# Performance work log

Measured on AMD Instinct MI355X. Metric: run time of the kernel, lower is better.

The kernel has to match this reference:

```python
import jax, jax.numpy as jnp
import numpy as np

B, L = 2, 5            # batches (scenes) and cavs per scene (fixed record_len)
THRESHOLD = 0.01       # communication threshold (eval path)
K_SIZE, SIGMA = 5, 1.0 # fixed gaussian smoothing filter


def _gaussian_kernel():
    c = K_SIZE // 2
    xx, yy = np.mgrid[0 - c:K_SIZE - c, 0 - c:K_SIZE - c]
    k = 1.0 / (2.0 * np.pi * SIGMA) * np.exp(-(np.square(xx) + np.square(yy)) / (2.0 * SIGMA ** 2))
    return jnp.asarray(k, jnp.float32)[None, None]  # OIHW (1,1,k,k)


def setup_inputs() -> dict:
    key = jax.random.key(0)
    ks = jax.random.split(key, 9)
    N, C, H, W, A = B * L, 64, 128, 256, 2
    return {
        "x": jax.random.normal(ks[0], (N, C, H, W), jnp.float32),
        "psm_single": jax.random.normal(ks[1], (N, A, H, W), jnp.float32),
        "inv_delay": jax.random.uniform(ks[2], (N,), jnp.float32, 0.1, 5.0),
        "ew_w": jax.random.normal(ks[3], (1,), jnp.float32),
        "ew_b": jax.random.normal(ks[4], (1,), jnp.float32),
        "ewc_w": jax.random.normal(ks[5], (1,), jnp.float32),
        "ewc_b": jax.random.normal(ks[6], (1,), jnp.float32),
        "sta_w1": jax.random.normal(ks[7], (4, 64), jnp.float32) * 0.1,
        "sta_w2": jax.random.normal(ks[8], (64, 4), jnp.float32) * 0.1,
    }


def reference(x, psm_single, inv_delay, ew_w, ew_b, ewc_w, ewc_b, sta_w1, sta_w2):
    N, C, H, W = x.shape
    dt = x.dtype

    # EnhanceWeight: per-cav AoI gate tanh(fc(1/(delay+0.1))) + 1
    enw = jnp.tanh(inv_delay * ew_w[0] + ew_b[0]) + 1.0          # (N,)
    x = x * enw[:, None, None, None]

    # Communication: sigmoid confidence, max over anchors, AoI gate, gaussian smooth
    conf = jax.nn.sigmoid(psm_single).max(axis=1, keepdims=True)  # (N,1,H,W)
    enc = jnp.tanh(inv_delay * ewc_w[0] + ewc_b[0]) + 1.0
    conf = conf * enc[:, None, None, None]
    conf = jax.lax.conv_general_dilated(
        conf, _gaussian_kernel().astype(dt), (1, 1), 'SAME',
        dimension_numbers=('NCHW', 'OIHW', 'NCHW'))
    mask = (conf > THRESHOLD).astype(dt)                          # (N,1,H,W)
    mask = mask.reshape(B, L, 1, H, W).at[:, 0].set(1.0)          # ego always communicates
    comm_rate = mask.mean()

    xm = x.reshape(B, L, C, H, W) * mask                          # masked per-cav features

    # TransformerFusion: per-pixel cross-agent attention, keep ego (row 0) output only
    feats = xm.transpose(0, 3, 4, 1, 2).reshape(B, H * W, L, C)   # (B, P, L, C)
    scale = 1.0 / jnp.sqrt(jnp.asarray(C, dt))
    scores = jnp.einsum('bpc,bplc->bpl', feats[:, :, 0], feats) * scale
    attn = jax.nn.softmax(scores, axis=-1)                        # (B, P, L)
    fused = jnp.einsum('bpl,bplc->bpc', attn, feats)              # (B, P, C)
    x_fuse = fused.transpose(0, 2, 1).reshape(B, C, H, W)

    # ShortTermAttention: channel gate from shared MLP over avg- and max-pooled stats
    def fc(v):  # v: (B, C)
        return jax.nn.relu(v @ sta_w1.T) @ sta_w2.T

    avg = x_fuse.mean(axis=(2, 3))
    mx = x_fuse.max(axis=(2, 3))
    gate = jax.nn.sigmoid(fc(avg) + fc(mx))                       # (B, C)
    out = x_fuse * gate[:, :, None, None]
    return out, comm_rate
```

## Files before the change

### kernel.cpp

```cpp
#include <hip/hip_runtime.h>
#include <math.h>

#define BB 2
#define LL 5
#define NN 10
#define CC 64
#define HH 128
#define WW 256
#define PP (HH*WW)
#define NP (NN*PP)


__global__ __launch_bounds__(256) void k_confmask(const float* __restrict__ psm,
                                                  const float* __restrict__ inv_delay,
                                                  const float* __restrict__ ewc_w,
                                                  const float* __restrict__ ewc_b,
                                                  float* __restrict__ mask,
                                                  float* __restrict__ cntp) {
    const float g0 = 0.15915494309189535f;
    const float g1 = 0.09653235263005391f;
    const float g2 = 0.05854983152431917f;
    const float g4 = 0.02153927930184936f;
    const float g5 = 0.01306423328468446f;
    const float g8 = 0.00291502449738744f;
    const float G[25] = { g8,g5,g4,g5,g8,
                          g5,g2,g1,g2,g5,
                          g4,g1,g0,g1,g4,
                          g5,g2,g1,g2,g5,
                          g8,g5,g4,g5,g8 };
    int blk = blockIdx.x;
    int n   = blk >> 7;
    int h   = blk & 127;
    int t   = threadIdx.x;
    float enc = tanhf(inv_delay[n] * ewc_w[0] + ewc_b[0]) + 1.0f;
    const float* pn0 = psm + (n * 2 + 0) * PP;
    const float* pn1 = psm + (n * 2 + 1) * PP;

    __shared__ float cs[5][WW];
#pragma unroll
    for (int r = 0; r < 5; ++r) {
        int row = h - 2 + r;
        float v = 0.0f;
        if ((unsigned)row < (unsigned)HH) {
            float a0 = pn0[row * WW + t];
            float a1 = pn1[row * WW + t];
            v = fmaxf(1.0f / (1.0f + expf(-a0)), 1.0f / (1.0f + expf(-a1))) * enc;
        }
        cs[r][t] = v;
    }
    __syncthreads();

    float acc = 0.0f;
#pragma unroll
    for (int r = 0; r < 5; ++r) {
#pragma unroll
        for (int dx = -2; dx <= 2; ++dx) {
            int col = t + dx;
            if ((unsigned)col < (unsigned)WW)
                acc += cs[r][col] * G[r * 5 + (dx + 2)];
        }
    }
    float mv = (acc > 0.01f) ? 1.0f : 0.0f;
    if ((n % LL) == 0) mv = 1.0f;
    mask[n * PP + h * WW + t] = mv;

    float v = mv;
#pragma unroll
    for (int o = 32; o > 0; o >>= 1) v += __shfl_down(v, o, 64);
    __shared__ float sred[4];
    int lane = t & 63, wid = t >> 6;
    if (lane == 0) sred[wid] = v;
    __syncthreads();
    if (t == 0) cntp[blk] = sred[0] + sred[1] + sred[2] + sred[3];
}

__global__ __launch_bounds__(256) void k_attnfuse(const float* __restrict__ x,
                                                  const float* __restrict__ mask,
                                                  const float* __restrict__ inv_delay,
                                                  const float* __restrict__ ew_w,
                                                  const float* __restrict__ ew_b,
                                                  float* __restrict__ out) {
    int blk = blockIdx.x;
    int b   = blk >> 9;
    int lane = threadIdx.x & 63;
    int wv   = threadIdx.x >> 6;
    int p = ((blk & 511) << 6) + lane;
    const float* xb = x + b * (LL * CC * PP) + p;
    int cbase = wv << 4;

    float xr[16][5];
    float s5[5] = {0.f, 0.f, 0.f, 0.f, 0.f};
#pragma unroll
    for (int cc = 0; cc < 16; ++cc) {
        const float* xc = xb + (cbase + cc) * PP;
#pragma unroll
        for (int l = 0; l < LL; ++l) xr[cc][l] = xc[l * CC * PP];
        float q = xr[cc][0];
#pragma unroll
        for (int l = 0; l < LL; ++l) s5[l] += q * xr[cc][l];
    }

    __shared__ float sred[4][5][64];
#pragma unroll
    for (int l = 0; l < LL; ++l) sred[wv][l][lane] = s5[l];
    __syncthreads();

    float ew0 = ew_w[0], eb0 = ew_b[0];
    float a[5];
    {
        float m[5], t[5], sc[5], e[5];
#pragma unroll
        for (int l = 0; l < LL; ++l) {
            t[l] = sred[0][l][lane] + sred[1][l][lane] + sred[2][l][lane] + sred[3][l][lane];
            float en = tanhf(inv_delay[b * LL + l] * ew0 + eb0) + 1.0f;
            m[l] = en * mask[(b * LL + l) * PP + p];
        }
        const float scale = 0.125f;
#pragma unroll
        for (int l = 0; l < LL; ++l) sc[l] = t[l] * m[0] * m[l] * scale;
        float mxv = fmaxf(fmaxf(fmaxf(sc[0], sc[1]), fmaxf(sc[2], sc[3])), sc[4]);
        float sum = 0.f;
#pragma unroll
        for (int l = 0; l < LL; ++l) { e[l] = expf(sc[l] - mxv); sum += e[l]; }
        float inv = 1.0f / sum;
#pragma unroll
        for (int l = 0; l < LL; ++l) a[l] = e[l] * inv * m[l];
    }

    float* ob = out + b * (CC * PP) + p;
#pragma unroll
    for (int cc = 0; cc < 16; ++cc) {
        float f = 0.f;
#pragma unroll
        for (int l = 0; l < LL; ++l) f += a[l] * xr[cc][l];
        ob[(cbase + cc) * PP] = f;
    }
}

__global__ void k_reduce(const float* __restrict__ xfuse,
                         float* __restrict__ avg_part,
                         float* __restrict__ mx_part) {
    int blk = blockIdx.x;
    int bc = blk >> 1;
    int half = blk & 1;
    const float4* row = (const float4*)(xfuse + bc * PP) + half * 4096;
    float s = 0.0f, m = -INFINITY;
    for (int i = threadIdx.x; i < 4096; i += 256) {
        float4 v = row[i];
        s += v.x + v.y + v.z + v.w;
        m = fmaxf(m, fmaxf(fmaxf(v.x, v.y), fmaxf(v.z, v.w)));
    }
#pragma unroll
    for (int o = 32; o > 0; o >>= 1) {
        s += __shfl_down(s, o, 64);
        m = fmaxf(m, __shfl_down(m, o, 64));
    }
    __shared__ float ss[4], sm[4];
    int lane = threadIdx.x & 63, wid = threadIdx.x >> 6;
    if (lane == 0) { ss[wid] = s; sm[wid] = m; }
    __syncthreads();
    if (threadIdx.x == 0) {
        avg_part[blk] = ss[0] + ss[1] + ss[2] + ss[3];
        mx_part[blk]  = fmaxf(fmaxf(sm[0], sm[1]), fmaxf(sm[2], sm[3]));
    }
}

__global__ __launch_bounds__(256) void k_scalegate(float* __restrict__ out,
                                                   const float* __restrict__ avg_part,
                                                   const float* __restrict__ mx_part,
                                                   const float* __restrict__ w1,
                                                   const float* __restrict__ w2,
                                                   const float* __restrict__ cntp) {
    int idx = blockIdx.x * 256 + threadIdx.x;
    int bc = idx >> 13;
    int b  = bc >> 6;
    int c  = bc & 63;
    __shared__ float hs[4];
    if (threadIdx.x < 4) {
        int j = threadIdx.x;
        float ha = 0.f, hm = 0.f;
        const float invP = 1.0f / (float)PP;
        for (int ch = 0; ch < CC; ++ch) {
            int i = (b * CC + ch) * 2;
            float av = (avg_part[i] + avg_part[i + 1]) * invP;
            float mv = fmaxf(mx_part[i], mx_part[i + 1]);
            float wv = w1[j * CC + ch];
            ha += av * wv;
            hm += mv * wv;
        }
        hs[j] = fmaxf(ha, 0.0f) + fmaxf(hm, 0.0f);
    }
    float4 v = ((float4*)out)[idx];
    __syncthreads();
    float g = hs[0] * w2[c * 4 + 0] + hs[1] * w2[c * 4 + 1]
            + hs[2] * w2[c * 4 + 2] + hs[3] * w2[c * 4 + 3];
    float gate = 1.0f / (1.0f + expf(-g));
    v.x *= gate; v.y *= gate; v.z *= gate; v.w *= gate;
    ((float4*)out)[idx] = v;

    if (blockIdx.x == 0) {
        float s = 0.0f;
        for (int j = threadIdx.x; j < 1280; j += 256) s += cntp[j];
#pragma unroll
        for (int o = 32; o > 0; o >>= 1) s += __shfl_down(s, o, 64);
        __shared__ float cs[4];
        int lane = threadIdx.x & 63, wid = threadIdx.x >> 6;
        if (lane == 0) cs[wid] = s;
        __syncthreads();
        if (threadIdx.x == 0)
            out[BB * CC * PP] = (cs[0] + cs[1] + cs[2] + cs[3]) * (1.0f / (float)NP);
    }
}

extern "C" void kernel_launch(void* const* d_in, const int* in_sizes, int n_in,
                              void* d_out, int out_size, void* d_ws, size_t ws_size,
                              hipStream_t stream) {
    const float* x         = (const float*)d_in[0];
    const float* psm       = (const float*)d_in[1];
    const float* inv_delay = (const float*)d_in[2];
    const float* ew_w      = (const float*)d_in[3];
    const float* ew_b      = (const float*)d_in[4];
    const float* ewc_w     = (const float*)d_in[5];
    const float* ewc_b     = (const float*)d_in[6];
    const float* w1        = (const float*)d_in[7];
    const float* w2        = (const float*)d_in[8];
    float* out = (float*)d_out;
    float* wsf = (float*)d_ws;

    float* avgp = wsf + 64;
    float* mxp  = wsf + 320;
    float* cntp = wsf + 576;
    float* mask = wsf + 4096;

    k_confmask<<<NN * HH, 256, 0, stream>>>(psm, inv_delay, ewc_w, ewc_b, mask, cntp);
    k_attnfuse<<<1024, 256, 0, stream>>>(x, mask, inv_delay, ew_w, ew_b, out);
    k_reduce<<<256, 256, 0, stream>>>(out, avgp, mxp);
    k_scalegate<<<BB * CC * PP / 4 / 256, 256, 0, stream>>>(out, avgp, mxp, w1, w2, cntp);
}
```

Before: 53.20 us.

## Fuse confidence mask and channel stats into attention kernel; split gate compute

Computes the gaussian-smoothed confidence mask for all five cavs directly inside the attention-fusion kernel using a shared-memory halo tile, which removes the mask buffer round trip and one launch. The same kernel also produces per-block channel sum and max partials through wave shuffles, so the separate pass that re-read the fused output for pooling is gone. A single-block finish kernel builds the gate and the comm rate, and a light scale kernel applies the gate. In exchange, psm halo regions are recomputed redundantly across blocks and each channel now pays a per-channel shuffle reduction.

Measured after the change: 56.10 us. 5.5% more time.

```diff
diff --git a/kernel.cpp b/kernel.cpp
--- a/kernel.cpp
+++ b/kernel.cpp
@@ -11,11 +11,16 @@
 #define NP (NN*PP)
 
 
-__global__ __launch_bounds__(256) void k_confmask(const float* __restrict__ psm,
+__global__ __launch_bounds__(256) void k_attnfuse(const float* __restrict__ x,
+                                                  const float* __restrict__ psm,
                                                   const float* __restrict__ inv_delay,
+                                                  const float* __restrict__ ew_w,
+                                                  const float* __restrict__ ew_b,
                                                   const float* __restrict__ ewc_w,
                                                   const float* __restrict__ ewc_b,
-                                                  float* __restrict__ mask,
+                                                  float* __restrict__ out,
+                                                  float* __restrict__ partS,
+                                                  float* __restrict__ partM,
                                                   float* __restrict__ cntp) {
     const float g0 = 0.15915494309189535f;
     const float g1 = 0.09653235263005391f;
@@ -28,63 +33,63 @@
                           g4,g1,g0,g1,g4,
                           g5,g2,g1,g2,g5,
                           g8,g5,g4,g5,g8 };
-    int blk = blockIdx.x;
-    int n   = blk >> 7;
-    int h   = blk & 127;
-    int t   = threadIdx.x;
-    float enc = tanhf(inv_delay[n] * ewc_w[0] + ewc_b[0]) + 1.0f;
-    const float* pn0 = psm + (n * 2 + 0) * PP;
-    const float* pn1 = psm + (n * 2 + 1) * PP;
-
-    __shared__ float cs[5][WW];
-#pragma unroll
-    for (int r = 0; r < 5; ++r) {
-        int row = h - 2 + r;
-        float v = 0.0f;
-        if ((unsigned)row < (unsigned)HH) {
-            float a0 = pn0[row * WW + t];
-            float a1 = pn1[row * WW + t];
-            v = fmaxf(1.0f / (1.0f + expf(-a0)), 1.0f / (1.0f + expf(-a1))) * enc;
-        }
-        cs[r][t] = v;
-    }
-    __syncthreads();
-
-    float acc = 0.0f;
-#pragma unroll
-    for (int r = 0; r < 5; ++r) {
-#pragma unroll
-        for (int dx = -2; dx <= 2; ++dx) {
-            int col = t + dx;
-            if ((unsigned)col < (unsigned)WW)
-                acc += cs[r][col] * G[r * 5 + (dx + 2)];
-        }
-    }
-    float mv = (acc > 0.01f) ? 1.0f : 0.0f;
-    if ((n % LL) == 0) mv = 1.0f;
-    mask[n * PP + h * WW + t] = mv;
-
-    float v = mv;
-#pragma unroll
-    for (int o = 32; o > 0; o >>= 1) v += __shfl_down(v, o, 64);
-    __shared__ float sred[4];
-    int lane = t & 63, wid = t >> 6;
-    if (lane == 0) sred[wid] = v;
-    __syncthreads();
-    if (t == 0) cntp[blk] = sred[0] + sred[1] + sred[2] + sred[3];
-}
-
-__global__ __launch_bounds__(256) void k_attnfuse(const float* __restrict__ x,
-                                                  const float* __restrict__ mask,
-                                                  const float* __restrict__ inv_delay,
-                                                  const float* __restrict__ ew_w,
-                                                  const float* __restrict__ ew_b,
-                                                  float* __restrict__ out) {
+
     int blk = blockIdx.x;
     int b   = blk >> 9;
-    int lane = threadIdx.x & 63;
-    int wv   = threadIdx.x >> 6;
-    int p = ((blk & 511) << 6) + lane;
+    int tid  = threadIdx.x;
+    int lane = tid & 63;
+    int wv   = tid >> 6;
+    int pblock = blk & 511;
+    int p = (pblock << 6) + lane;
+    int h  = pblock >> 2;
+    int c0 = (pblock & 3) << 6;
+
+    __shared__ float cs[5 * 5 * 68];
+    __shared__ float encs[5], enws[5];
+    if (tid < 5)
+        encs[tid] = tanhf(inv_delay[b * LL + tid] * ewc_w[0] + ewc_b[0]) + 1.0f;
+    else if (tid < 10)
+        enws[tid - 5] = tanhf(inv_delay[b * LL + tid - 5] * ew_w[0] + ew_b[0]) + 1.0f;
+    __syncthreads();
+
+    for (int idx = tid; idx < 1700; idx += 256) {
+        int l   = idx / 340;
+        int rem = idx - l * 340;
+        int r   = rem / 68;
+        int cc2 = rem - r * 68;
+        int row = h - 2 + r;
+        int col = c0 - 2 + cc2;
+        float v = 0.0f;
+        if ((unsigned)row < (unsigned)HH && (unsigned)col < (unsigned)WW) {
+            int n = b * LL + l;
+            float a0 = psm[(n * 2 + 0) * PP + row * WW + col];
+            float a1 = psm[(n * 2 + 1) * PP + row * WW + col];
+            v = fmaxf(1.0f / (1.0f + expf(-a0)), 1.0f / (1.0f + expf(-a1))) * encs[l];
+        }
+        cs[idx] = v;
+    }
+    __syncthreads();
+
+    float mv[5];
+#pragma unroll
+    for (int l = 0; l < LL; ++l) {
+        float acc = 0.0f;
+#pragma unroll
+        for (int r = 0; r < 5; ++r)
+#pragma unroll
+            for (int dx = 0; dx < 5; ++dx)
+                acc += cs[l * 340 + r * 68 + lane + dx] * G[r * 5 + dx];
+        mv[l] = (acc > 0.01f) ? 1.0f : 0.0f;
+    }
+    mv[0] = 1.0f;
+
+    if (wv == 0) {
+        float v = mv[0] + mv[1] + mv[2] + mv[3] + mv[4];
+#pragma unroll
+        for (int o = 32; o > 0; o >>= 1) v += __shfl_down(v, o, 64);
+        if (lane == 0) cntp[blk] = v;
+    }
+
     const float* xb = x + b * (LL * CC * PP) + p;
     int cbase = wv << 4;
 
@@ -105,15 +110,13 @@
     for (int l = 0; l < LL; ++l) sred[wv][l][lane] = s5[l];
     __syncthreads();
 
-    float ew0 = ew_w[0], eb0 = ew_b[0];
     float a[5];
     {
         float m[5], t[5], sc[5], e[5];
 #pragma unroll
         for (int l = 0; l < LL; ++l) {
             t[l] = sred[0][l][lane] + sred[1][l][lane] + sred[2][l][lane] + sred[3][l][lane];
-            float en = tanhf(inv_delay[b * LL + l] * ew0 + eb0) + 1.0f;
-            m[l] = en * mask[(b * LL + l) * PP + p];
+            m[l] = enws[l] * mv[l];
         }
         const float scale = 0.125f;
 #pragma unroll
@@ -134,82 +137,87 @@
 #pragma unroll
         for (int l = 0; l < LL; ++l) f += a[l] * xr[cc][l];
         ob[(cbase + cc) * PP] = f;
-    }
-}
-
-__global__ void k_reduce(const float* __restrict__ xfuse,
-                         float* __restrict__ avg_part,
-                         float* __restrict__ mx_part) {
-    int blk = blockIdx.x;
-    int bc = blk >> 1;
-    int half = blk & 1;
-    const float4* row = (const float4*)(xfuse + bc * PP) + half * 4096;
-    float s = 0.0f, m = -INFINITY;
-    for (int i = threadIdx.x; i < 4096; i += 256) {
-        float4 v = row[i];
-        s += v.x + v.y + v.z + v.w;
-        m = fmaxf(m, fmaxf(fmaxf(v.x, v.y), fmaxf(v.z, v.w)));
-    }
-#pragma unroll
-    for (int o = 32; o > 0; o >>= 1) {
-        s += __shfl_down(s, o, 64);
-        m = fmaxf(m, __shfl_down(m, o, 64));
-    }
-    __shared__ float ss[4], sm[4];
-    int lane = threadIdx.x & 63, wid = threadIdx.x >> 6;
-    if (lane == 0) { ss[wid] = s; sm[wid] = m; }
-    __syncthreads();
-    if (threadIdx.x == 0) {
-        avg_part[blk] = ss[0] + ss[1] + ss[2] + ss[3];
-        mx_part[blk]  = fmaxf(fmaxf(sm[0], sm[1]), fmaxf(sm[2], sm[3]));
-    }
-}
-
-__global__ __launch_bounds__(256) void k_scalegate(float* __restrict__ out,
-                                                   const float* __restrict__ avg_part,
-                                                   const float* __restrict__ mx_part,
-                                                   const float* __restrict__ w1,
-                                                   const float* __restrict__ w2,
-                                                   const float* __restrict__ cntp) {
+
+        float sv = f, mm = f;
+#pragma unroll
+        for (int o = 1; o < 64; o <<= 1) {
+            sv += __shfl_xor(sv, o, 64);
+            mm = fmaxf(mm, __shfl_xor(mm, o, 64));
+        }
+        if (lane == 0) {
+            partS[blk * CC + cbase + cc] = sv;
+            partM[blk * CC + cbase + cc] = mm;
+        }
+    }
+}
+
+__global__ __launch_bounds__(256) void k_finish(const float* __restrict__ partS,
+                                                const float* __restrict__ partM,
+                                                const float* __restrict__ cntp,
+                                                const float* __restrict__ w1,
+                                                const float* __restrict__ w2,
+                                                float* __restrict__ gate,
+                                                float* __restrict__ comm_out) {
+    int t = threadIdx.x;
+    int pair = t >> 1;
+    int sub  = t & 1;
+    __shared__ float sS[2][128], sM[2][128];
+    {
+        int b = pair >> 6, c = pair & 63;
+        float s = 0.f, m = -INFINITY;
+        int base = b * 512 + sub * 256;
+        for (int pb = 0; pb < 256; ++pb) {
+            int i = (base + pb) * CC + c;
+            s += partS[i];
+            m = fmaxf(m, partM[i]);
+        }
+        sS[sub][pair] = s;
+        sM[sub][pair] = m;
+    }
+    __syncthreads();
+    __shared__ float stA[128], stM[128];
+    if (t < 128) {
+        stA[t] = (sS[0][t] + sS[1][t]) * (1.0f / (float)PP);
+        stM[t] = fmaxf(sM[0][t], sM[1][t]);
+    }
+    __syncthreads();
+    __shared__ float hs[BB][4];
+    if (t < BB * 4) {
+        int b = t >> 2, j = t & 3;
+        float ha = 0.f, hm = 0.f;
+        for (int c = 0; c < CC; ++c) {
+            float wv = w1[j * CC + c];
+            ha += stA[b * CC + c] * wv;
+            hm += stM[b * CC + c] * wv;
+        }
+        hs[b][j] = fmaxf(ha, 0.0f) + fmaxf(hm, 0.0f);
+    }
+    __syncthreads();
+    if (t < 128) {
+        int b = t >> 6, c = t & 63;
+        float g = hs[b][0] * w2[c * 4 + 0] + hs[b][1] * w2[c * 4 + 1]
+                + hs[b][2] * w2[c * 4 + 2] + hs[b][3] * w2[c * 4 + 3];
+        gate[t] = 1.0f / (1.0f + expf(-g));
+    }
+    float s = 0.f;
+    for (int j = t; j < 1024; j += 256) s += cntp[j];
+#pragma unroll
+    for (int o = 32; o > 0; o >>= 1) s += __shfl_down(s, o, 64);
+    __shared__ float cred[4];
+    if ((t & 63) == 0) cred[t >> 6] = s;
+    __syncthreads();
+    if (t == 0)
+        comm_out[0] = (cred[0] + cred[1] + cred[2] + cred[3]) * (1.0f / (float)NP);
+}
+
+__global__ __launch_bounds__(256) void k_scale(float* __restrict__ out,
+                                               const float* __restrict__ gate) {
     int idx = blockIdx.x * 256 + threadIdx.x;
     int bc = idx >> 13;
-    int b  = bc >> 6;
-    int c  = bc & 63;
-    __shared__ float hs[4];
-    if (threadIdx.x < 4) {
-        int j = threadIdx.x;
-        float ha = 0.f, hm = 0.f;
-        const float invP = 1.0f / (float)PP;
-        for (int ch = 0; ch < CC; ++ch) {
-            int i = (b * CC + ch) * 2;
-            float av = (avg_part[i] + avg_part[i + 1]) * invP;
-            float mv = fmaxf(mx_part[i], mx_part[i + 1]);
-            float wv = w1[j * CC + ch];
-            ha += av * wv;
-            hm += mv * wv;
-        }
-        hs[j] = fmaxf(ha, 0.0f) + fmaxf(hm, 0.0f);
-    }
+    float g = gate[bc];
     float4 v = ((float4*)out)[idx];
-    __syncthreads();
-    float g = hs[0] * w2[c * 4 + 0] + hs[1] * w2[c * 4 + 1]
-            + hs[2] * w2[c * 4 + 2] + hs[3] * w2[c * 4 + 3];
-    float gate = 1.0f / (1.0f + expf(-g));
-    v.x *= gate; v.y *= gate; v.z *= gate; v.w *= gate;
+    v.x *= g; v.y *= g; v.z *= g; v.w *= g;
     ((float4*)out)[idx] = v;
-
-    if (blockIdx.x == 0) {
-        float s = 0.0f;
-        for (int j = threadIdx.x; j < 1280; j += 256) s += cntp[j];
-#pragma unroll
-        for (int o = 32; o > 0; o >>= 1) s += __shfl_down(s, o, 64);
-        __shared__ float cs[4];
-        int lane = threadIdx.x & 63, wid = threadIdx.x >> 6;
-        if (lane == 0) cs[wid] = s;
-        __syncthreads();
-        if (threadIdx.x == 0)
-            out[BB * CC * PP] = (cs[0] + cs[1] + cs[2] + cs[3]) * (1.0f / (float)NP);
-    }
 }
 
 extern "C" void kernel_launch(void* const* d_in, const int* in_sizes, int n_in,
@@ -227,13 +235,13 @@
     float* out = (float*)d_out;
     float* wsf = (float*)d_ws;
 
-    float* avgp = wsf + 64;
-    float* mxp  = wsf + 320;
-    float* cntp = wsf + 576;
-    float* mask = wsf + 4096;
-
-    k_confmask<<<NN * HH, 256, 0, stream>>>(psm, inv_delay, ewc_w, ewc_b, mask, cntp);
-    k_attnfuse<<<1024, 256, 0, stream>>>(x, mask, inv_delay, ew_w, ew_b, out);
-    k_reduce<<<256, 256, 0, stream>>>(out, avgp, mxp);
-    k_scalegate<<<BB * CC * PP / 4 / 256, 256, 0, stream>>>(out, avgp, mxp, w1, w2, cntp);
-}
+    float* gate  = wsf;
+    float* cntp  = wsf + 128;
+    float* partS = wsf + 2048;
+    float* partM = wsf + 2048 + 1024 * CC;
+
+    k_attnfuse<<<1024, 256, 0, stream>>>(x, psm, inv_delay, ew_w, ew_b, ewc_w, ewc_b,
+                                         out, partS, partM, cntp);
+    k_finish<<<1, 256, 0, stream>>>(partS, partM, cntp, w1, w2, gate, out + BB * CC * PP);
+    k_scale<<<BB * CC * PP / 4 / 256, 256, 0, stream>>>(out, gate);
+}
```
